# Optimization experiments

Hardware: AMD Instinct MI355X
Metric: run time of the kernel (lower is better)

Reference implementation:

```python
import jax, jax.numpy as jnp
import numpy as np

EPS = 1e-4

def _gauss(length, mean, logstd):
    # (F,K,length) Gaussian kernel on symmetric coord in [-1,1]
    coord = jnp.linspace(-1.0, 1.0, length)
    std = jnp.exp(logstd)
    return jnp.exp(-0.5 * ((coord[None, None, :] - mean[..., None]) / std[..., None]) ** 2)

def _expk(length, logtau):
    # (F,K,length) exponential-decay kernel on coord [0,1,...]
    coord = jnp.arange(length, dtype=jnp.float32)
    tau = jnp.exp(logtau) + 1e-4
    return jnp.exp(-coord[None, None, :] / tau[..., None])

def setup_inputs():
    key = jax.random.key(0)
    ks = jax.random.split(key, 11)
    B, F, K = 16, 4, 16
    Y, X, P, T = 16, 16, 16, 8
    return {
        'fieldpatch': jax.random.normal(ks[0], (B, F, Y, X, P, T), jnp.float32),
        'dareapatch': jax.random.uniform(ks[1], (B, Y, X), jnp.float32, 0.5, 1.5),
        'dlevpatch': jax.random.uniform(ks[2], (B, P), jnp.float32, 0.5, 1.5),
        'dtimepatch': jax.random.uniform(ks[3], (B, T), jnp.float32, 0.5, 1.5),
        'lat_mean': 0.1 * jax.random.normal(ks[4], (F, K), jnp.float32),
        'lat_logstd': 0.1 * jax.random.normal(ks[5], (F, K), jnp.float32),
        'lon_mean': 0.1 * jax.random.normal(ks[6], (F, K), jnp.float32),
        'lon_logstd': 0.1 * jax.random.normal(ks[7], (F, K), jnp.float32),
        'lev_mean': 0.1 * jax.random.normal(ks[8], (F, K), jnp.float32),
        'lev_logstd': 0.1 * jax.random.normal(ks[9], (F, K), jnp.float32),
        'time_logtau': 0.1 * jax.random.normal(ks[10], (F, K), jnp.float32),
    }

def reference(fieldpatch, dareapatch, dlevpatch, dtimepatch,
              lat_mean, lat_logstd, lon_mean, lon_logstd,
              lev_mean, lev_logstd, time_logtau):
    B, F, Y, X, P, T = fieldpatch.shape
    # batch-mean quadrature weights used for kernel normalization
    dareamean = dareapatch.mean(axis=0)   # (Y,X)
    dlevmean = dlevpatch.mean(axis=0)     # (P,)
    dtimemean = dtimepatch.mean(axis=0)   # (T,)
    # separable parametric kernel: outer product of 1D kernels -> (F,K,Y,X,P,T)
    klat = _gauss(Y, lat_mean, lat_logstd)
    klon = _gauss(X, lon_mean, lon_logstd)
    klev = _gauss(P, lev_mean, lev_logstd)
    ktime = _expk(T, time_logtau)
    kernel = (klat[:, :, :, None, None, None]
              * klon[:, :, None, :, None, None]
              * klev[:, :, None, None, :, None]
              * ktime[:, :, None, None, None, :])
    # normalize: all four dims are kerneled, so norm = darea*dlev*dtime
    norm = (dareamean[:, :, None, None]
            * dlevmean[None, None, :, None]
            * dtimemean[None, None, None, :])   # (Y,X,P,T)
    integral = jnp.einsum('fkyxpt,yxpt->fk', kernel, norm) + EPS
    weights = kernel / integral[:, :, None, None, None, None]
    # integrate: per-sample quadrature weights, contract all kerneled dims
    quad = (dareapatch[:, :, :, None, None]
            * dlevpatch[:, None, None, :, None]
            * dtimepatch[:, None, None, None, :])   # (B,Y,X,P,T)
    feats = jnp.einsum('bfyxpt,fkyxpt,byxpt->bfk', fieldpatch, weights, quad)
    return feats.reshape(B, -1)   # (B, F*K)
```

## Files before the change

### kernel.cpp

```cpp
#include <hip/hip_runtime.h>
#include <math.h>

#define Bn 16
#define Fn 4
#define Kn 16
#define Yn 16
#define Xn 16
#define Pn 16
#define Tn 8

__global__ __launch_bounds__(1024) void pkl_kernel(
    const float* __restrict__ field,
    const float* __restrict__ darea,
    const float* __restrict__ dlev,
    const float* __restrict__ dtime,
    const float* __restrict__ lat_mean, const float* __restrict__ lat_logstd,
    const float* __restrict__ lon_mean, const float* __restrict__ lon_logstd,
    const float* __restrict__ lev_mean, const float* __restrict__ lev_logstd,
    const float* __restrict__ time_logtau,
    float* __restrict__ out)
{
    __shared__ float s_dareamean[Yn*Xn];
    __shared__ float s_klat[Kn*Yn], s_klon[Kn*Xn], s_klev[Kn*Pn], s_ktime[Kn*Tn];
    __shared__ float s_dlevmean[Pn], s_dtimemean[Tn];
    __shared__ float s_darea_b[Yn*Xn], s_dlev_b[Pn], s_dtime_b[Tn];
    __shared__ float s_part[Kn*Yn];
    __shared__ float s_inv[Kn];
    __shared__ float s_red[16][Kn];

    const int tid = threadIdx.x;
    const int bf  = blockIdx.x;
    const int b   = bf >> 2;
    const int f   = bf & 3;

    if (tid < 256) {
        float s = 0.f;
        #pragma unroll
        for (int bb = 0; bb < Bn; ++bb) s += darea[bb*(Yn*Xn) + tid];
        s_dareamean[tid] = s * (1.f/16.f);
    } else if (tid < 512) {
        int i = tid - 256; int k = i >> 4; int y = i & 15;
        float m  = lat_mean[f*Kn + k];
        float sd = expf(lat_logstd[f*Kn + k]);
        float c  = -1.f + (float)y * (2.f/15.f);
        float z  = (c - m) / sd;
        s_klat[i] = expf(-0.5f * z * z);
    } else if (tid < 768) {
        int i = tid - 512; int k = i >> 4; int x = i & 15;
        float m  = lon_mean[f*Kn + k];
        float sd = expf(lon_logstd[f*Kn + k]);
        float c  = -1.f + (float)x * (2.f/15.f);
        float z  = (c - m) / sd;
        s_klon[i] = expf(-0.5f * z * z);
    } else {
        int i = tid - 768; int k = i >> 4; int p = i & 15;
        float m  = lev_mean[f*Kn + k];
        float sd = expf(lev_logstd[f*Kn + k]);
        float c  = -1.f + (float)p * (2.f/15.f);
        float z  = (c - m) / sd;
        s_klev[i] = expf(-0.5f * z * z);
    }
    if (tid < 128) {
        int k = tid >> 3; int t = tid & 7;
        float tau = expf(time_logtau[f*Kn + k]) + 1e-4f;
        s_ktime[tid] = expf(-(float)t / tau);
    } else if (tid < 144) {
        int p = tid - 128;
        float s = 0.f;
        #pragma unroll
        for (int bb = 0; bb < Bn; ++bb) s += dlev[bb*Pn + p];
        s_dlevmean[p] = s * (1.f/16.f);
    } else if (tid < 152) {
        int t = tid - 144;
        float s = 0.f;
        #pragma unroll
        for (int bb = 0; bb < Bn; ++bb) s += dtime[bb*Tn + t];
        s_dtimemean[t] = s * (1.f/16.f);
    } else if (tid < 168) {
        int p = tid - 152;
        s_dlev_b[p] = dlev[b*Pn + p];
    } else if (tid < 176) {
        int t = tid - 168;
        s_dtime_b[t] = dtime[b*Tn + t];
    } else if (tid < 432) {
        int i = tid - 176;
        s_darea_b[i] = darea[b*(Yn*Xn) + i];
    }
    __syncthreads();

    if (tid < 256) {
        int k = tid >> 4; int y = tid & 15;
        float s = 0.f;
        #pragma unroll
        for (int x = 0; x < Xn; ++x) s += s_klon[k*Xn + x] * s_dareamean[y*Xn + x];
        s_part[tid] = s_klat[k*Yn + y] * s;
    }
    __syncthreads();
    if (tid < Kn) {
        int k = tid;
        float sa = 0.f;
        #pragma unroll
        for (int y = 0; y < Yn; ++y) sa += s_part[k*Yn + y];
        float sl = 0.f;
        #pragma unroll
        for (int p = 0; p < Pn; ++p) sl += s_klev[k*Pn + p] * s_dlevmean[p];
        float st = 0.f;
        #pragma unroll
        for (int t = 0; t < Tn; ++t) st += s_ktime[k*Tn + t] * s_dtimemean[t];
        s_inv[k] = 1.f / (sa * sl * st + 1e-4f);
    }
    __syncthreads();

    const int yx = tid >> 2;
    const int pq = tid & 3;
    const int y  = yx >> 4;
    const int x  = yx & 15;

    const float da = s_darea_b[yx];
    float dt[Tn];
    #pragma unroll
    for (int t = 0; t < Tn; ++t) dt[t] = s_dtime_b[t];

    const float4* fptr = (const float4*)(field + (size_t)bf * (Yn*Xn*Pn*Tn) + (size_t)tid * 32);
    float w[4][Tn];
    #pragma unroll
    for (int pp = 0; pp < 4; ++pp) {
        float dl = s_dlev_b[pq*4 + pp] * da;
        float4 v0 = fptr[pp*2 + 0];
        float4 v1 = fptr[pp*2 + 1];
        w[pp][0] = v0.x * (dt[0] * dl);
        w[pp][1] = v0.y * (dt[1] * dl);
        w[pp][2] = v0.z * (dt[2] * dl);
        w[pp][3] = v0.w * (dt[3] * dl);
        w[pp][4] = v1.x * (dt[4] * dl);
        w[pp][5] = v1.y * (dt[5] * dl);
        w[pp][6] = v1.z * (dt[6] * dl);
        w[pp][7] = v1.w * (dt[7] * dl);
    }

    float acc[Kn];
    for (int k = 0; k < Kn; ++k) {
        float kt[Tn];
        #pragma unroll
        for (int t = 0; t < Tn; ++t) kt[t] = s_ktime[k*Tn + t];
        float s = 0.f;
        #pragma unroll
        for (int pp = 0; pp < 4; ++pp) {
            float tp = 0.f;
            #pragma unroll
            for (int t = 0; t < Tn; ++t) tp += w[pp][t] * kt[t];
            s += tp * s_klev[k*Pn + pq*4 + pp];
        }
        acc[k] = s * s_klat[k*Yn + y] * s_klon[k*Xn + x];
    }

    #pragma unroll
    for (int k = 0; k < Kn; ++k) {
        float v = acc[k];
        #pragma unroll
        for (int off = 32; off > 0; off >>= 1) v += __shfl_xor(v, off, 64);
        acc[k] = v;
    }
    const int wave = tid >> 6;
    const int lane = tid & 63;
    if (lane == 0) {
        #pragma unroll
        for (int k = 0; k < Kn; ++k) s_red[wave][k] = acc[k];
    }
    __syncthreads();
    if (tid < Kn) {
        float s = 0.f;
        #pragma unroll
        for (int wv = 0; wv < 16; ++wv) s += s_red[wv][tid];
        out[b*(Fn*Kn) + f*Kn + tid] = s * s_inv[tid];
    }
}

extern "C" void kernel_launch(void* const* d_in, const int* in_sizes, int n_in,
                              void* d_out, int out_size, void* d_ws, size_t ws_size,
                              hipStream_t stream) {
    const float* field      = (const float*)d_in[0];
    const float* darea      = (const float*)d_in[1];
    const float* dlev       = (const float*)d_in[2];
    const float* dtime      = (const float*)d_in[3];
    const float* lat_mean   = (const float*)d_in[4];
    const float* lat_logstd = (const float*)d_in[5];
    const float* lon_mean   = (const float*)d_in[6];
    const float* lon_logstd = (const float*)d_in[7];
    const float* lev_mean   = (const float*)d_in[8];
    const float* lev_logstd = (const float*)d_in[9];
    const float* time_logtau= (const float*)d_in[10];
    float* out = (float*)d_out;

    pkl_kernel<<<Bn*Fn, 1024, 0, stream>>>(
        field, darea, dlev, dtime,
        lat_mean, lat_logstd, lon_mean, lon_logstd,
        lev_mean, lev_logstd, time_logtau, out);
}
```

Baseline: 89.21 us.

## Split each (b,f) block into four y-quarter blocks with atomic output accumulation

Launches four times as many blocks of 256 threads, each covering a quarter of the Y range for one (b,f) pair. Partial sums are combined with atomicAdd into an output zeroed by a memset. This spreads 64 large blocks across more compute units to raise occupancy and parallelism. In exchange each block redundantly recomputes the kernel tables and normalization, and it adds a memset launch and atomics.

Result: faster. 84.64 us (-5.1%).

```diff
diff --git a/kernel.cpp b/kernel.cpp
--- a/kernel.cpp
+++ b/kernel.cpp
@@ -9,7 +9,7 @@
 #define Pn 16
 #define Tn 8
 
-__global__ __launch_bounds__(1024) void pkl_kernel(
+__global__ __launch_bounds__(256) void pkl_kernel(
     const float* __restrict__ field,
     const float* __restrict__ darea,
     const float* __restrict__ dlev,
@@ -23,42 +23,46 @@
     __shared__ float s_dareamean[Yn*Xn];
     __shared__ float s_klat[Kn*Yn], s_klon[Kn*Xn], s_klev[Kn*Pn], s_ktime[Kn*Tn];
     __shared__ float s_dlevmean[Pn], s_dtimemean[Tn];
-    __shared__ float s_darea_b[Yn*Xn], s_dlev_b[Pn], s_dtime_b[Tn];
+    __shared__ float s_darea_b[4*Xn];
+    __shared__ float s_dlev_b[Pn], s_dtime_b[Tn];
     __shared__ float s_part[Kn*Yn];
     __shared__ float s_inv[Kn];
-    __shared__ float s_red[16][Kn];
+    __shared__ float s_red[4][Kn];
 
     const int tid = threadIdx.x;
-    const int bf  = blockIdx.x;
+    const int blk = blockIdx.x;
+    const int bf  = blk >> 2;
+    const int yq  = blk & 3;
     const int b   = bf >> 2;
     const int f   = bf & 3;
 
-    if (tid < 256) {
+    {
         float s = 0.f;
         #pragma unroll
         for (int bb = 0; bb < Bn; ++bb) s += darea[bb*(Yn*Xn) + tid];
         s_dareamean[tid] = s * (1.f/16.f);
-    } else if (tid < 512) {
-        int i = tid - 256; int k = i >> 4; int y = i & 15;
-        float m  = lat_mean[f*Kn + k];
-        float sd = expf(lat_logstd[f*Kn + k]);
-        float c  = -1.f + (float)y * (2.f/15.f);
-        float z  = (c - m) / sd;
-        s_klat[i] = expf(-0.5f * z * z);
-    } else if (tid < 768) {
-        int i = tid - 512; int k = i >> 4; int x = i & 15;
-        float m  = lon_mean[f*Kn + k];
-        float sd = expf(lon_logstd[f*Kn + k]);
-        float c  = -1.f + (float)x * (2.f/15.f);
-        float z  = (c - m) / sd;
-        s_klon[i] = expf(-0.5f * z * z);
-    } else {
-        int i = tid - 768; int k = i >> 4; int p = i & 15;
-        float m  = lev_mean[f*Kn + k];
-        float sd = expf(lev_logstd[f*Kn + k]);
-        float c  = -1.f + (float)p * (2.f/15.f);
-        float z  = (c - m) / sd;
-        s_klev[i] = expf(-0.5f * z * z);
+
+        const int k = tid >> 4;
+        const int i = tid & 15;
+        const float c = -1.f + (float)i * (2.f/15.f);
+        {
+            float m  = lat_mean[f*Kn + k];
+            float sd = expf(lat_logstd[f*Kn + k]);
+            float z  = (c - m) / sd;
+            s_klat[tid] = expf(-0.5f * z * z);
+        }
+        {
+            float m  = lon_mean[f*Kn + k];
+            float sd = expf(lon_logstd[f*Kn + k]);
+            float z  = (c - m) / sd;
+            s_klon[tid] = expf(-0.5f * z * z);
+        }
+        {
+            float m  = lev_mean[f*Kn + k];
+            float sd = expf(lev_logstd[f*Kn + k]);
+            float z  = (c - m) / sd;
+            s_klev[tid] = expf(-0.5f * z * z);
+        }
     }
     if (tid < 128) {
         int k = tid >> 3; int t = tid & 7;
@@ -82,13 +86,13 @@
     } else if (tid < 176) {
         int t = tid - 168;
         s_dtime_b[t] = dtime[b*Tn + t];
-    } else if (tid < 432) {
+    } else if (tid < 240) {
         int i = tid - 176;
-        s_darea_b[i] = darea[b*(Yn*Xn) + i];
-    }
-    __syncthreads();
-
-    if (tid < 256) {
+        s_darea_b[i] = darea[b*(Yn*Xn) + yq*(4*Xn) + i];
+    }
+    __syncthreads();
+
+    {
         int k = tid >> 4; int y = tid & 15;
         float s = 0.f;
         #pragma unroll
@@ -111,17 +115,19 @@
     }
     __syncthreads();
 
-    const int yx = tid >> 2;
-    const int pq = tid & 3;
-    const int y  = yx >> 4;
-    const int x  = yx & 15;
-
-    const float da = s_darea_b[yx];
+    const int y_local = tid >> 6;
+    const int x       = (tid >> 2) & 15;
+    const int pq      = tid & 3;
+    const int y       = yq*4 + y_local;
+
+    const float da = s_darea_b[(y_local << 4) | x];
     float dt[Tn];
     #pragma unroll
     for (int t = 0; t < Tn; ++t) dt[t] = s_dtime_b[t];
 
-    const float4* fptr = (const float4*)(field + (size_t)bf * (Yn*Xn*Pn*Tn) + (size_t)tid * 32);
+    const float4* fptr = (const float4*)(field + (size_t)bf * (Yn*Xn*Pn*Tn)
+                                               + (size_t)yq * (4*Xn*Pn*Tn)
+                                               + (size_t)tid * 32);
     float w[4][Tn];
     #pragma unroll
     for (int pp = 0; pp < 4; ++pp) {
@@ -169,10 +175,8 @@
     }
     __syncthreads();
     if (tid < Kn) {
-        float s = 0.f;
-        #pragma unroll
-        for (int wv = 0; wv < 16; ++wv) s += s_red[wv][tid];
-        out[b*(Fn*Kn) + f*Kn + tid] = s * s_inv[tid];
+        float s = s_red[0][tid] + s_red[1][tid] + s_red[2][tid] + s_red[3][tid];
+        atomicAdd(&out[bf*Kn + tid], s * s_inv[tid]);
     }
 }
 
@@ -192,7 +196,9 @@
     const float* time_logtau= (const float*)d_in[10];
     float* out = (float*)d_out;
 
-    pkl_kernel<<<Bn*Fn, 1024, 0, stream>>>(
+    hipMemsetAsync(out, 0, (size_t)out_size * sizeof(float), stream);
+
+    pkl_kernel<<<Bn*Fn*4, 256, 0, stream>>>(
         field, darea, dlev, dtime,
         lat_mean, lat_logstd, lon_mean, lon_logstd,
         lev_mean, lev_logstd, time_logtau, out);
```
